# Kernel tuning notes

Hardware: AMD Instinct MI355X
Metric: run time of the kernel (lower is better)

## Reference

```python
import jax, jax.numpy as jnp
import numpy as np

H = 128      # hidden_dim
D = 256      # 2*hidden_dim (transformer d_model)
NH = 4       # attention heads
EPS = 1e-5

def _bn(x, g, b):
    # BatchNorm1d, training mode: batch statistics over node axis (biased var)
    mu = x.mean(0)
    var = x.var(0)
    return (x - mu) / jnp.sqrt(var + EPS) * g + b

def _ln(x, g, b):
    mu = x.mean(-1, keepdims=True)
    var = x.var(-1, keepdims=True)
    return (x - mu) / jnp.sqrt(var + EPS) * g + b

def _sage(x_src, x_dst, src, dst, Wl, bl, Wr):
    # PyG SAGEConv(aggr='mean'): lin_l(mean_j x_src[src_j]) + lin_r(x_dst); lin_r has no bias
    n_dst = x_dst.shape[0]
    msg = x_src[src]  # [E, H] gather
    agg = jnp.zeros((n_dst, msg.shape[-1]), msg.dtype).at[dst].add(msg)
    cnt = jnp.zeros((n_dst,), msg.dtype).at[dst].add(1.0)
    agg = agg / jnp.maximum(cnt, 1.0)[:, None]
    return agg @ Wl + bl + x_dst @ Wr


def setup_inputs() -> dict:
    key = jax.random.key(0)
    T, NU, NT, FU, FT = 12, 10000, 2500, 64, 32
    E_tt, E_ut, E_tu = 50000, 100000, 100000
    L, TL, FFN = 3, 3, 256
    ks = iter(jax.random.split(key, 64))
    def nrm(shape, s=0.05):
        return jax.random.normal(next(ks), shape, jnp.float32) * s
    inp = {
        'x_user': nrm((T, NU, FU), 1.0),
        'x_tag': nrm((T, NT, FT), 1.0),
        'edge_tt': jax.random.randint(next(ks), (T, 2, E_tt), 0, NT),
        'edge_ut_src': jax.random.randint(next(ks), (T, E_ut), 0, NU),
        'edge_ut_dst': jax.random.randint(next(ks), (T, E_ut), 0, NT),
        'edge_tu_src': jax.random.randint(next(ks), (T, E_tu), 0, NT),
        'edge_tu_dst': jax.random.randint(next(ks), (T, E_tu), 0, NU),
        'bn_user_g': jnp.ones((FU,)), 'bn_user_b': jnp.zeros((FU,)),
        'bn_tag_g': jnp.ones((FT,)), 'bn_tag_b': jnp.zeros((FT,)),
        'proj_user_W': nrm((FU, H)), 'proj_user_b': jnp.zeros((H,)),
        'proj_tag_W': nrm((FT, H)), 'proj_tag_b': jnp.zeros((H,)),
        # conv params: axis0 = conv layer (3), axis1 = edge type (0:tt, 1:ut, 2:tu)
        'conv_Wl': nrm((L, 3, H, H)), 'conv_bl': jnp.zeros((L, 3, H)),
        'conv_Wr': nrm((L, 3, H, H)),
        'attn_Wq': nrm((TL, D, D)), 'attn_bq': jnp.zeros((TL, D)),
        'attn_Wk': nrm((TL, D, D)), 'attn_bk': jnp.zeros((TL, D)),
        'attn_Wv': nrm((TL, D, D)), 'attn_bv': jnp.zeros((TL, D)),
        'attn_Wo': nrm((TL, D, D)), 'attn_bo': jnp.zeros((TL, D)),
        'ln1_g': jnp.ones((TL, D)), 'ln1_b': jnp.zeros((TL, D)),
        'ffn_W1': nrm((TL, D, FFN)), 'ffn_b1': jnp.zeros((TL, FFN)),
        'ffn_W2': nrm((TL, FFN, D)), 'ffn_b2': jnp.zeros((TL, D)),
        'ln2_g': jnp.ones((TL, D)), 'ln2_b': jnp.zeros((TL, D)),
        'head_W': nrm((D, 4)), 'head_b': jnp.zeros((4,)),
    }
    return inp


def reference(x_user, x_tag, edge_tt, edge_ut_src, edge_ut_dst, edge_tu_src, edge_tu_dst,
              bn_user_g, bn_user_b, bn_tag_g, bn_tag_b,
              proj_user_W, proj_user_b, proj_tag_W, proj_tag_b,
              conv_Wl, conv_bl, conv_Wr,
              attn_Wq, attn_bq, attn_Wk, attn_bk, attn_Wv, attn_bv, attn_Wo, attn_bo,
              ln1_g, ln1_b, ffn_W1, ffn_b1, ffn_W2, ffn_b2, ln2_g, ln2_b,
              head_W, head_b):
    def month(xu, xt, e_tt, eus, eud, ets, etd):
        xu = _bn(xu, bn_user_g, bn_user_b) @ proj_user_W + proj_user_b
        xt = _bn(xt, bn_tag_g, bn_tag_b) @ proj_tag_W + proj_tag_b
        for l in range(conv_Wl.shape[0]):
            o_tt = _sage(xt, xt, e_tt[0], e_tt[1], conv_Wl[l, 0], conv_bl[l, 0], conv_Wr[l, 0])
            o_ut = _sage(xu, xt, eus, eud, conv_Wl[l, 1], conv_bl[l, 1], conv_Wr[l, 1])
            o_tu = _sage(xt, xu, ets, etd, conv_Wl[l, 2], conv_bl[l, 2], conv_Wr[l, 2])
            # HeteroConv aggr='mean': tag receives 2 relations, user receives 1
            xt = jax.nn.relu((o_tt + o_ut) * 0.5)
            xu = jax.nn.relu(o_tu)
        return jnp.concatenate([xu.mean(0), xt.mean(0)])  # [2H]

    emb = jax.vmap(month)(x_user, x_tag, edge_tt, edge_ut_src, edge_ut_dst,
                          edge_tu_src, edge_tu_dst)  # [12, 2H]
    x = emb[None]  # [1, 12, D]
    B, S, Dm = x.shape
    dh = Dm // NH
    scale = 1.0 / jnp.sqrt(jnp.float32(dh))
    for l in range(attn_Wq.shape[0]):
        q = (x @ attn_Wq[l] + attn_bq[l]).reshape(B, S, NH, dh)
        k = (x @ attn_Wk[l] + attn_bk[l]).reshape(B, S, NH, dh)
        v = (x @ attn_Wv[l] + attn_bv[l]).reshape(B, S, NH, dh)
        a = jax.nn.softmax(jnp.einsum('bqhd,bkhd->bhqk', q, k) * scale, axis=-1)
        o = jnp.einsum('bhqk,bkhd->bqhd', a, v).reshape(B, S, Dm) @ attn_Wo[l] + attn_bo[l]
        x = _ln(x + o, ln1_g[l], ln1_b[l])          # post-norm (norm_first=False)
        f = jax.nn.relu(x @ ffn_W1[l] + ffn_b1[l]) @ ffn_W2[l] + ffn_b2[l]
        x = _ln(x + f, ln2_g[l], ln2_b[l])
    # predictions: columns = [qpd, answer_rate, retention, growth]
    return x[:, -1, :] @ head_W + head_b  # [1, 4]
```

## Files before the change

### kernel.cpp

```cpp
#include <hip/hip_runtime.h>

constexpr int T = 12;
constexpr int NU = 10000;
constexpr int NT = 2500;
constexpr int FU = 64;
constexpr int FT = 32;
constexpr int H = 128;
constexpr int D = 256;
constexpr int E_TT = 50000;
constexpr int E_UT = 100000;
constexpr int E_TU = 100000;
constexpr float EPS = 1e-5f;

__global__ __launch_bounds__(256) void bnsum_kernel(
    const float* __restrict__ x, int N, int F, float* __restrict__ sum,
    float* __restrict__ sq, int bpm) {
  int m = blockIdx.x / bpm, bc = blockIdx.x % bpm;
  int g = 256 / F;
  int c = threadIdx.x % F, rg = threadIdx.x / F;
  int rows = (N + bpm - 1) / bpm;
  int lo = bc * rows, hi = min(N, lo + rows);
  float s = 0.f, q = 0.f;
  for (int r = lo + rg; r < hi; r += g) {
    float v = x[((long)m * N + r) * F + c];
    s += v; q += v * v;
  }
  __shared__ float ssm[256], qsm[256];
  ssm[threadIdx.x] = s; qsm[threadIdx.x] = q;
  __syncthreads();
  if (rg == 0) {
    for (int i = 1; i < g; ++i) { s += ssm[i * F + c]; q += qsm[i * F + c]; }
    atomicAdd(&sum[m * F + c], s);
    atomicAdd(&sq[m * F + c], q);
  }
}

template <int F>
__global__ __launch_bounds__(128) void proj_kernel(
    const float* __restrict__ x, const float* __restrict__ sum, const float* __restrict__ sq,
    const float* __restrict__ g, const float* __restrict__ b,
    const float* __restrict__ W, const float* __restrict__ pb,
    float* __restrict__ out, int N, int chunks) {
  constexpr int RPB = 8;
  int m = blockIdx.x / chunks, chunk = blockIdx.x % chunks;
  int row0 = chunk * RPB;
  int nr = min(RPB, N - row0);
  int c = threadIdx.x;
  __shared__ __align__(16) float Ws[F][H];
  __shared__ __align__(16) float A[RPB][F];
  __shared__ float scv[F], shv[F];
  for (int k = 0; k < F; ++k) Ws[k][c] = W[k * H + c];
  if (c < F) {
    float mu = sum[m * F + c] * (1.f / N);
    float var = sq[m * F + c] * (1.f / N) - mu * mu;
    float inv = rsqrtf(var + EPS);
    float s = g[c] * inv;
    scv[c] = s; shv[c] = b[c] - mu * s;
  }
  __syncthreads();
  const float* xb = x + ((long)m * N + row0) * F;
  for (int i = c; i < nr * F; i += 128) {
    int kk = i % F;
    A[i / F][kk] = xb[i] * scv[kk] + shv[kk];
  }
  __syncthreads();
  float acc[RPB];
#pragma unroll
  for (int r = 0; r < RPB; ++r) acc[r] = 0.f;
  for (int k = 0; k < F; k += 4) {
    float w0 = Ws[k][c], w1 = Ws[k + 1][c], w2 = Ws[k + 2][c], w3 = Ws[k + 3][c];
#pragma unroll
    for (int r = 0; r < RPB; ++r) {
      float4 a = *(const float4*)&A[r][k];
      acc[r] += a.x * w0 + a.y * w1 + a.z * w2 + a.w * w3;
    }
  }
  float bias = pb[c];
  float* ob = out + ((long)m * N + row0) * H;
  for (int r = 0; r < nr; ++r) ob[r * H + c] = acc[r] + bias;
}

__global__ __launch_bounds__(256) void count_kernel(
    const int* __restrict__ dst, long mstride, int E, int* __restrict__ cnt, int N) {
  long idx = (long)blockIdx.x * 256 + threadIdx.x;
  if (idx >= (long)T * E) return;
  int m = (int)(idx / E), e = (int)(idx % E);
  int d = dst[m * mstride + e];
  atomicAdd(&cnt[m * N + d], 1);
}

__global__ __launch_bounds__(1024) void scan_kernel(
    int* __restrict__ iw, long cnt_tt, long off_tt, long cur_tt,
    long cnt_ut, long off_ut, long cur_ut,
    long cnt_tu, long off_tu, long cur_tu) {
  int b = blockIdx.x;
  int type = b / 12, m = b % 12;
  const int* cnt; int* off; int* cur; int N;
  if (type == 0) {
    cnt = iw + cnt_tt + (long)m * NT; off = iw + off_tt + (long)m * (NT + 1);
    cur = iw + cur_tt + (long)m * NT; N = NT;
  } else if (type == 1) {
    cnt = iw + cnt_ut + (long)m * NT; off = iw + off_ut + (long)m * (NT + 1);
    cur = iw + cur_ut + (long)m * NT; N = NT;
  } else {
    cnt = iw + cnt_tu + (long)m * NU; off = iw + off_tu + (long)m * (NU + 1);
    cur = iw + cur_tu + (long)m * NU; N = NU;
  }
  __shared__ int s[1024];
  int tid = threadIdx.x;
  int running = 0;
  for (int base = 0; base < N; base += 1024) {
    int i = base + tid;
    int v = (i < N) ? cnt[i] : 0;
    s[tid] = v;
    __syncthreads();
    for (int o = 1; o < 1024; o <<= 1) {
      int t = (tid >= o) ? s[tid - o] : 0;
      __syncthreads();
      s[tid] += t;
      __syncthreads();
    }
    if (i < N) { int e = running + s[tid] - v; off[i] = e; cur[i] = e; }
    int tot = s[1023];
    __syncthreads();
    running += tot;
  }
  if (tid == 0) off[N] = running;
}

__global__ __launch_bounds__(256) void fill_kernel(
    const int* __restrict__ src, long sstride, const int* __restrict__ dst, long dstride,
    int E, int* __restrict__ cur, int N, int* __restrict__ srcs) {
  long idx = (long)blockIdx.x * 256 + threadIdx.x;
  if (idx >= (long)T * E) return;
  int m = (int)(idx / E), e = (int)(idx % E);
  int d = dst[m * dstride + e];
  int sv = src[m * sstride + e];
  int pos = atomicAdd(&cur[m * N + d], 1);
  srcs[(long)m * E + pos] = sv;
}

__global__ __launch_bounds__(256) void agg_kernel(
    const int* __restrict__ off, const int* __restrict__ srcs,
    const float* __restrict__ xsrc, float* __restrict__ agg,
    int Ndst, int Nsrc, int E, int chunks) {
  int m = blockIdx.x / chunks, chunk = blockIdx.x % chunks;
  int slot = threadIdx.x >> 5;
  int c4 = (threadIdx.x & 31) * 4;
  int row = chunk * 8 + slot;
  if (row >= Ndst) return;
  const int* o = off + (long)m * (Ndst + 1);
  int o0 = o[row], o1 = o[row + 1];
  const int* sp = srcs + (long)m * E;
  const float* xb = xsrc + (long)m * Nsrc * H;
  float4 acc = {0.f, 0.f, 0.f, 0.f};
  for (int j = o0; j < o1; ++j) {
    float4 v = *(const float4*)&xb[(long)sp[j] * H + c4];
    acc.x += v.x; acc.y += v.y; acc.z += v.z; acc.w += v.w;
  }
  float inv = 1.f / (float)max(o1 - o0, 1);
  acc.x *= inv; acc.y *= inv; acc.z *= inv; acc.w *= inv;
  *(float4*)&agg[((long)m * Ndst + row) * H + c4] = acc;
}

__global__ __launch_bounds__(128) void update_tag_kernel(
    float* __restrict__ xt, const float* __restrict__ aggtt, const float* __restrict__ aggut,
    const float* __restrict__ Wl, const float* __restrict__ bl, const float* __restrict__ Wr,
    int layer, int chunks) {
  constexpr int RPB = 16;
  int m = blockIdx.x / chunks, chunk = blockIdx.x % chunks;
  int row0 = chunk * RPB;
  int nr = min(RPB, NT - row0);
  int c = threadIdx.x;
  __shared__ __align__(16) float sm0[RPB][H], sm1[RPB][H], sm2[RPB][H];
  const float* p0 = aggtt + ((long)m * NT + row0) * H;
  const float* p1 = xt + ((long)m * NT + row0) * H;
  const float* p2 = aggut + ((long)m * NT + row0) * H;
  for (int r = 0; r < nr; ++r) {
    sm0[r][c] = p0[r * H + c];
    sm1[r][c] = p1[r * H + c];
    sm2[r][c] = p2[r * H + c];
  }
  __syncthreads();
  const float* wl0 = Wl + (long)(layer * 3 + 0) * H * H;
  const float* wr0 = Wr + (long)(layer * 3 + 0) * H * H;
  const float* wl1 = Wl + (long)(layer * 3 + 1) * H * H;
  const float* wr1 = Wr + (long)(layer * 3 + 1) * H * H;
  float acc[RPB];
#pragma unroll
  for (int r = 0; r < RPB; ++r) acc[r] = 0.f;
  for (int k = 0; k < H; k += 4) {
    float a0[4], a1[4], a2[4];
#pragma unroll
    for (int u = 0; u < 4; ++u) {
      a0[u] = wl0[(k + u) * H + c];
      a1[u] = wr0[(k + u) * H + c] + wr1[(k + u) * H + c];
      a2[u] = wl1[(k + u) * H + c];
    }
#pragma unroll
    for (int r = 0; r < RPB; ++r) {
      float4 v0 = *(const float4*)&sm0[r][k];
      float4 v1 = *(const float4*)&sm1[r][k];
      float4 v2 = *(const float4*)&sm2[r][k];
      acc[r] += v0.x * a0[0] + v0.y * a0[1] + v0.z * a0[2] + v0.w * a0[3]
              + v1.x * a1[0] + v1.y * a1[1] + v1.z * a1[2] + v1.w * a1[3]
              + v2.x * a2[0] + v2.y * a2[1] + v2.z * a2[2] + v2.w * a2[3];
    }
  }
  float bias = bl[(layer * 3 + 0) * H + c] + bl[(layer * 3 + 1) * H + c];
  float* ob = xt + ((long)m * NT + row0) * H;
  for (int r = 0; r < nr; ++r) ob[r * H + c] = fmaxf(0.f, 0.5f * (acc[r] + bias));
}

__global__ __launch_bounds__(128) void update_user_kernel(
    float* __restrict__ xu, const float* __restrict__ aggtu,
    const float* __restrict__ Wl, const float* __restrict__ bl, const float* __restrict__ Wr,
    int layer, int chunks) {
  constexpr int RPB = 16;
  int m = blockIdx.x / chunks, chunk = blockIdx.x % chunks;
  int row0 = chunk * RPB;
  int nr = min(RPB, NU - row0);
  int c = threadIdx.x;
  __shared__ __align__(16) float sm0[RPB][H], sm1[RPB][H];
  const float* p0 = aggtu + ((long)m * NU + row0) * H;
  const float* p1 = xu + ((long)m * NU + row0) * H;
  for (int r = 0; r < nr; ++r) {
    sm0[r][c] = p0[r * H + c];
    sm1[r][c] = p1[r * H + c];
  }
  __syncthreads();
  const float* wl = Wl + (long)(layer * 3 + 2) * H * H;
  const float* wr = Wr + (long)(layer * 3 + 2) * H * H;
  float acc[RPB];
#pragma unroll
  for (int r = 0; r < RPB; ++r) acc[r] = 0.f;
  for (int k = 0; k < H; k += 4) {
    float a0[4], a1[4];
#pragma unroll
    for (int u = 0; u < 4; ++u) {
      a0[u] = wl[(k + u) * H + c];
      a1[u] = wr[(k + u) * H + c];
    }
#pragma unroll
    for (int r = 0; r < RPB; ++r) {
      float4 v0 = *(const float4*)&sm0[r][k];
      float4 v1 = *(const float4*)&sm1[r][k];
      acc[r] += v0.x * a0[0] + v0.y * a0[1] + v0.z * a0[2] + v0.w * a0[3]
              + v1.x * a1[0] + v1.y * a1[1] + v1.z * a1[2] + v1.w * a1[3];
    }
  }
  float bias = bl[(layer * 3 + 2) * H + c];
  float* ob = xu + ((long)m * NU + row0) * H;
  for (int r = 0; r < nr; ++r) ob[r * H + c] = fmaxf(0.f, acc[r] + bias);
}

__global__ __launch_bounds__(256) void pool_kernel(
    const float* __restrict__ x, int N, float* __restrict__ emb, int base, int bpm) {
  int m = blockIdx.x / bpm, bc = blockIdx.x % bpm;
  int c = threadIdx.x & 127, rg = threadIdx.x >> 7;
  int rows = (N + bpm - 1) / bpm;
  int lo = bc * rows, hi = min(N, lo + rows);
  float acc = 0.f;
  for (int r = lo + rg; r < hi; r += 2) acc += x[((long)m * N + r) * H + c];
  __shared__ float smem[2][H];
  smem[rg][c] = acc;
  __syncthreads();
  if (threadIdx.x < H) {
    atomicAdd(&emb[m * D + base + c], (smem[0][c] + smem[1][c]) * (1.f / N));
  }
}

__device__ __forceinline__ void fma4(float4& a, const float4 x, const float4 w0,
                                     const float4 w1, const float4 w2, const float4 w3) {
  a.x += x.x * w0.x + x.y * w1.x + x.z * w2.x + x.w * w3.x;
  a.y += x.x * w0.y + x.y * w1.y + x.z * w2.y + x.w * w3.y;
  a.z += x.x * w0.z + x.y * w1.z + x.z * w2.z + x.w * w3.z;
  a.w += x.x * w0.w + x.y * w1.w + x.z * w2.w + x.w * w3.w;
}

__device__ __forceinline__ void mm_slice(const float (&Xs)[12][256], const float* __restrict__ W,
                                         int ks, int tid, float* __restrict__ pOut) {
  int cg = tid & 63, rg = tid >> 6;
  int c4 = cg * 4;
  int s0 = rg * 3;
  float4 a0 = {0, 0, 0, 0}, a1 = {0, 0, 0, 0}, a2 = {0, 0, 0, 0};
  for (int k = ks * 64; k < ks * 64 + 64; k += 4) {
    float4 w0 = *(const float4*)&W[(k + 0) * 256 + c4];
    float4 w1 = *(const float4*)&W[(k + 1) * 256 + c4];
    float4 w2 = *(const float4*)&W[(k + 2) * 256 + c4];
    float4 w3 = *(const float4*)&W[(k + 3) * 256 + c4];
    fma4(a0, *(const float4*)&Xs[s0 + 0][k], w0, w1, w2, w3);
    fma4(a1, *(const float4*)&Xs[s0 + 1][k], w0, w1, w2, w3);
    fma4(a2, *(const float4*)&Xs[s0 + 2][k], w0, w1, w2, w3);
  }
  *(float4*)&pOut[(s0 + 0) * 256 + c4] = a0;
  *(float4*)&pOut[(s0 + 1) * 256 + c4] = a1;
  *(float4*)&pOut[(s0 + 2) * 256 + c4] = a2;
}

__device__ __forceinline__ void ln_rows(float (&Xs)[12][256], const float* __restrict__ g,
                                        const float* __restrict__ b, float (&rs)[4],
                                        float (&rq)[4], int tid) {
  for (int s = 0; s < 12; ++s) {
    float v = Xs[s][tid];
    float sm_ = v, sq_ = v * v;
    for (int o = 32; o > 0; o >>= 1) {
      sm_ += __shfl_down(sm_, o);
      sq_ += __shfl_down(sq_, o);
    }
    if ((tid & 63) == 0) { rs[tid >> 6] = sm_; rq[tid >> 6] = sq_; }
    __syncthreads();
    float mu = (rs[0] + rs[1] + rs[2] + rs[3]) * (1.f / 256);
    float var = (rq[0] + rq[1] + rq[2] + rq[3]) * (1.f / 256) - mu * mu;
    Xs[s][tid] = (v - mu) * rsqrtf(var + EPS) * g[tid] + b[tid];
    __syncthreads();
  }
}

__global__ __launch_bounds__(256) void trans_qkv(
    const float* __restrict__ xb, const float* __restrict__ pF2, const float* __restrict__ x1v,
    const float* __restrict__ b2, const float* __restrict__ ln2g, const float* __restrict__ ln2b,
    float* __restrict__ xb_out,
    const float* __restrict__ Wq, const float* __restrict__ Wk, const float* __restrict__ Wv,
    float* __restrict__ pQKV, int fuse) {
  __shared__ float Xs[12][256];
  __shared__ float rs[4], rq[4];
  int tid = threadIdx.x;
  int mat = blockIdx.x >> 2, ks = blockIdx.x & 3;
  if (fuse) {
    for (int s = 0; s < 12; ++s) {
      int i = s * 256 + tid;
      Xs[s][tid] = pF2[i] + pF2[3072 + i] + pF2[6144 + i] + pF2[9216 + i] + b2[tid] + x1v[i];
    }
    __syncthreads();
    ln_rows(Xs, ln2g, ln2b, rs, rq, tid);
    if (blockIdx.x == 0)
      for (int s = 0; s < 12; ++s) xb_out[s * 256 + tid] = Xs[s][tid];
  } else {
    for (int s = 0; s < 12; ++s) Xs[s][tid] = xb[s * 256 + tid];
    __syncthreads();
  }
  const float* W = (mat == 0) ? Wq : (mat == 1) ? Wk : Wv;
  mm_slice(Xs, W, ks, tid, pQKV + (mat * 4 + ks) * 3072);
}

__global__ __launch_bounds__(256) void trans_attn(
    const float* __restrict__ pQKV, const float* __restrict__ bq,
    const float* __restrict__ bk, const float* __restrict__ bv, float* __restrict__ O) {
  __shared__ float Qs[12][256], Ksh[12][256], Vs[12][256];
  __shared__ float Sc[4][12][12];
  int tid = threadIdx.x;
  for (int s = 0; s < 12; ++s) {
    int i = s * 256 + tid;
    const float* p = pQKV;
    Qs[s][tid] = p[i] + p[3072 + i] + p[6144 + i] + p[9216 + i] + bq[tid];
    p = pQKV + 12288;
    Ksh[s][tid] = p[i] + p[3072 + i] + p[6144 + i] + p[9216 + i] + bk[tid];
    p = pQKV + 24576;
    Vs[s][tid] = p[i] + p[3072 + i] + p[6144 + i] + p[9216 + i] + bv[tid];
  }
  __syncthreads();
  for (int idx = tid; idx < 576; idx += 256) {
    int h = idx / 144, rem = idx % 144, qi = rem / 12, ti = rem % 12;
    float acc = 0.f;
    for (int d = 0; d < 64; d += 4) {
      float4 qv = *(const float4*)&Qs[qi][h * 64 + d];
      float4 kv = *(const float4*)&Ksh[ti][h * 64 + d];
      acc += qv.x * kv.x + qv.y * kv.y + qv.z * kv.z + qv.w * kv.w;
    }
    Sc[h][qi][ti] = acc * 0.125f;
  }
  __syncthreads();
  if (tid < 48) {
    int h = tid / 12, qi = tid % 12;
    float mx = -1e30f;
    for (int t2 = 0; t2 < 12; ++t2) mx = fmaxf(mx, Sc[h][qi][t2]);
    float e[12], sum = 0.f;
    for (int t2 = 0; t2 < 12; ++t2) { e[t2] = __expf(Sc[h][qi][t2] - mx); sum += e[t2]; }
    float inv = 1.f / sum;
    for (int t2 = 0; t2 < 12; ++t2) Sc[h][qi][t2] = e[t2] * inv;
  }
  __syncthreads();
  int h = tid >> 6;
#pragma unroll
  for (int s = 0; s < 12; ++s) {
    float acc = 0.f;
#pragma unroll
    for (int t2 = 0; t2 < 12; ++t2) acc += Sc[h][s][t2] * Vs[t2][tid];
    O[s * 256 + tid] = acc;
  }
}

__global__ __launch_bounds__(256) void trans_mm(
    const float* __restrict__ In, const float* __restrict__ W, float* __restrict__ pOut) {
  __shared__ float Xs[12][256];
  int tid = threadIdx.x, ks = blockIdx.x;
  for (int s = 0; s < 12; ++s) Xs[s][tid] = In[s * 256 + tid];
  __syncthreads();
  mm_slice(Xs, W, ks, tid, pOut + ks * 3072);
}

__global__ __launch_bounds__(256) void trans_ffn1(
    const float* __restrict__ pP, const float* __restrict__ bo, const float* __restrict__ xb,
    const float* __restrict__ ln1g, const float* __restrict__ ln1b, float* __restrict__ x1_out,
    const float* __restrict__ W1, float* __restrict__ pF1) {
  __shared__ float Xs[12][256];
  __shared__ float rs[4], rq[4];
  int tid = threadIdx.x, ks = blockIdx.x;
  for (int s = 0; s < 12; ++s) {
    int i = s * 256 + tid;
    Xs[s][tid] = pP[i] + pP[3072 + i] + pP[6144 + i] + pP[9216 + i] + bo[tid] + xb[i];
  }
  __syncthreads();
  ln_rows(Xs, ln1g, ln1b, rs, rq, tid);
  if (ks == 0)
    for (int s = 0; s < 12; ++s) x1_out[s * 256 + tid] = Xs[s][tid];
  mm_slice(Xs, W1, ks, tid, pF1 + ks * 3072);
}

__global__ __launch_bounds__(256) void trans_ffn2(
    const float* __restrict__ pF1, const float* __restrict__ b1,
    const float* __restrict__ W2, float* __restrict__ pF2) {
  __shared__ float Xs[12][256];
  int tid = threadIdx.x, ks = blockIdx.x;
  for (int s = 0; s < 12; ++s) {
    int i = s * 256 + tid;
    Xs[s][tid] = fmaxf(0.f, pF1[i] + pF1[3072 + i] + pF1[6144 + i] + pF1[9216 + i] + b1[tid]);
  }
  __syncthreads();
  mm_slice(Xs, W2, ks, tid, pF2 + ks * 3072);
}

__global__ __launch_bounds__(256) void trans_head(
    const float* __restrict__ pF2, const float* __restrict__ b2, const float* __restrict__ x1v,
    const float* __restrict__ ln2g, const float* __restrict__ ln2b,
    const float* __restrict__ hW, const float* __restrict__ hb, float* __restrict__ out) {
  __shared__ float h[256];
  __shared__ float rs[4], rq[4];
  int tid = threadIdx.x;
  int i = 11 * 256 + tid;
  float v = pF2[i] + pF2[3072 + i] + pF2[6144 + i] + pF2[9216 + i] + b2[tid] + x1v[i];
  float sm_ = v, sq_ = v * v;
  for (int o = 32; o > 0; o >>= 1) { sm_ += __shfl_down(sm_, o); sq_ += __shfl_down(sq_, o); }
  if ((tid & 63) == 0) { rs[tid >> 6] = sm_; rq[tid >> 6] = sq_; }
  __syncthreads();
  float mu = (rs[0] + rs[1] + rs[2] + rs[3]) * (1.f / 256);
  float var = (rq[0] + rq[1] + rq[2] + rq[3]) * (1.f / 256) - mu * mu;
  h[tid] = (v - mu) * rsqrtf(var + EPS) * ln2g[tid] + ln2b[tid];
  __syncthreads();
  if (tid < 4) {
    float acc = hb[tid];
    for (int k = 0; k < 256; ++k) acc += h[k] * hW[k * 4 + tid];
    out[tid] = acc;
  }
}

extern "C" void kernel_launch(void* const* d_in, const int* in_sizes, int n_in,
                              void* d_out, int out_size, void* d_ws, size_t ws_size,
                              hipStream_t stream) {
  (void)in_sizes; (void)n_in; (void)out_size; (void)ws_size;
  const float* x_user = (const float*)d_in[0];
  const float* x_tag  = (const float*)d_in[1];
  const int* edge_tt  = (const int*)d_in[2];
  const int* e_us     = (const int*)d_in[3];
  const int* e_ud     = (const int*)d_in[4];
  const int* e_ts     = (const int*)d_in[5];
  const int* e_td     = (const int*)d_in[6];
  const float* bn_ug  = (const float*)d_in[7];
  const float* bn_ub  = (const float*)d_in[8];
  const float* bn_tg  = (const float*)d_in[9];
  const float* bn_tb  = (const float*)d_in[10];
  const float* pu_W   = (const float*)d_in[11];
  const float* pu_b   = (const float*)d_in[12];
  const float* pt_W   = (const float*)d_in[13];
  const float* pt_b   = (const float*)d_in[14];
  const float* cWl    = (const float*)d_in[15];
  const float* cbl    = (const float*)d_in[16];
  const float* cWr    = (const float*)d_in[17];
  const float* aWq    = (const float*)d_in[18];
  const float* abq    = (const float*)d_in[19];
  const float* aWk    = (const float*)d_in[20];
  const float* abk    = (const float*)d_in[21];
  const float* aWv    = (const float*)d_in[22];
  const float* abv    = (const float*)d_in[23];
  const float* aWo    = (const float*)d_in[24];
  const float* abo    = (const float*)d_in[25];
  const float* l1g    = (const float*)d_in[26];
  const float* l1b    = (const float*)d_in[27];
  const float* fW1    = (const float*)d_in[28];
  const float* fb1    = (const float*)d_in[29];
  const float* fW2    = (const float*)d_in[30];
  const float* fb2    = (const float*)d_in[31];
  const float* l2g    = (const float*)d_in[32];
  const float* l2b    = (const float*)d_in[33];
  const float* hW     = (const float*)d_in[34];
  const float* hb     = (const float*)d_in[35];

  float* ws = (float*)d_ws;
  int* iw = (int*)d_ws;
  size_t o = 0;
  auto alloc = [&](size_t n) { size_t r = o; o += n; return r; };
  size_t sum_u = alloc(T * FU), sq_u = alloc(T * FU);
  size_t sum_t = alloc(T * FT), sq_t = alloc(T * FT);
  size_t cnt_tt = alloc((size_t)T * NT), cnt_ut = alloc((size_t)T * NT), cnt_tu = alloc((size_t)T * NU);
  size_t emb = alloc(T * D);
  size_t zeroElems = o;
  size_t off_tt = alloc((size_t)T * (NT + 1)), off_ut = alloc((size_t)T * (NT + 1)), off_tu = alloc((size_t)T * (NU + 1));
  size_t cur_tt = alloc((size_t)T * NT), cur_ut = alloc((size_t)T * NT), cur_tu = alloc((size_t)T * NU);
  size_t srcs_tt = alloc((size_t)T * E_TT), srcs_ut = alloc((size_t)T * E_UT), srcs_tu = alloc((size_t)T * E_TU);
  size_t xu = alloc((size_t)T * NU * H), xt = alloc((size_t)T * NT * H);
  size_t agg_tt = alloc((size_t)T * NT * H), agg_ut = alloc((size_t)T * NT * H), agg_tu = alloc((size_t)T * NU * H);

  size_t pQKV = cnt_tt;
  size_t pP   = cnt_tt + 36864;
  size_t pF1  = cnt_tt + 49152;
  size_t pF2  = cnt_tt + 61440;
  size_t Ob   = cnt_tt + 73728;
  size_t x1b  = cnt_tt + 76800;

  hipMemsetAsync(d_ws, 0, zeroElems * sizeof(float), stream);

  bnsum_kernel<<<dim3(T * 8), 256, 0, stream>>>(x_user, NU, FU, ws + sum_u, ws + sq_u, 8);
  bnsum_kernel<<<dim3(T * 4), 256, 0, stream>>>(x_tag, NT, FT, ws + sum_t, ws + sq_t, 4);
  proj_kernel<FU><<<dim3(T * ((NU + 7) / 8)), 128, 0, stream>>>(
      x_user, ws + sum_u, ws + sq_u, bn_ug, bn_ub, pu_W, pu_b, ws + xu, NU, (NU + 7) / 8);
  proj_kernel<FT><<<dim3(T * ((NT + 7) / 8)), 128, 0, stream>>>(
      x_tag, ws + sum_t, ws + sq_t, bn_tg, bn_tb, pt_W, pt_b, ws + xt, NT, (NT + 7) / 8);
  count_kernel<<<dim3((T * E_TT + 255) / 256), 256, 0, stream>>>(edge_tt + E_TT, 2L * E_TT, E_TT, iw + cnt_tt, NT);
  count_kernel<<<dim3((T * E_UT + 255) / 256), 256, 0, stream>>>(e_ud, E_UT, E_UT, iw + cnt_ut, NT);
  count_kernel<<<dim3((T * E_TU + 255) / 256), 256, 0, stream>>>(e_td, E_TU, E_TU, iw + cnt_tu, NU);
  scan_kernel<<<dim3(36), 1024, 0, stream>>>(iw, (long)cnt_tt, (long)off_tt, (long)cur_tt,
                                             (long)cnt_ut, (long)off_ut, (long)cur_ut,
                                             (long)cnt_tu, (long)off_tu, (long)cur_tu);
  fill_kernel<<<dim3((T * E_TT + 255) / 256), 256, 0, stream>>>(edge_tt, 2L * E_TT, edge_tt + E_TT, 2L * E_TT, E_TT, iw + cur_tt, NT, iw + srcs_tt);
  fill_kernel<<<dim3((T * E_UT + 255) / 256), 256, 0, stream>>>(e_us, E_UT, e_ud, E_UT, E_UT, iw + cur_ut, NT, iw + srcs_ut);
  fill_kernel<<<dim3((T * E_TU + 255) / 256), 256, 0, stream>>>(e_ts, E_TU, e_td, E_TU, E_TU, iw + cur_tu, NU, iw + srcs_tu);
  int ch_t = (NT + 7) / 8, ch_u = (NU + 7) / 8;
  for (int l = 0; l < 3; ++l) {
    agg_kernel<<<dim3(T * ch_t), 256, 0, stream>>>(iw + off_tt, iw + srcs_tt, ws + xt, ws + agg_tt, NT, NT, E_TT, ch_t);
    agg_kernel<<<dim3(T * ch_t), 256, 0, stream>>>(iw + off_ut, iw + srcs_ut, ws + xu, ws + agg_ut, NT, NU, E_UT, ch_t);
    agg_kernel<<<dim3(T * ch_u), 256, 0, stream>>>(iw + off_tu, iw + srcs_tu, ws + xt, ws + agg_tu, NU, NT, E_TU, ch_u);
    update_tag_kernel<<<dim3(T * ((NT + 15) / 16)), 128, 0, stream>>>(ws + xt, ws + agg_tt, ws + agg_ut, cWl, cbl, cWr, l, (NT + 15) / 16);
    update_user_kernel<<<dim3(T * ((NU + 15) / 16)), 128, 0, stream>>>(ws + xu, ws + agg_tu, cWl, cbl, cWr, l, (NU + 15) / 16);
  }
  pool_kernel<<<dim3(T * 8), 256, 0, stream>>>(ws + xu, NU, ws + emb, 0, 8);
  pool_kernel<<<dim3(T * 2), 256, 0, stream>>>(ws + xt, NT, ws + emb, H, 2);
  long DD = (long)D * D;
  for (int l = 0; l < 3; ++l) {
    int fuse = (l > 0);
    int lp = fuse ? (l - 1) : 0;
    trans_qkv<<<dim3(12), 256, 0, stream>>>(
        ws + emb, ws + pF2, ws + x1b, fb2 + lp * D, l2g + lp * D, l2b + lp * D, ws + emb,
        aWq + l * DD, aWk + l * DD, aWv + l * DD, ws + pQKV, fuse);
    trans_attn<<<dim3(1), 256, 0, stream>>>(ws + pQKV, abq + l * D, abk + l * D, abv + l * D, ws + Ob);
    trans_mm<<<dim3(4), 256, 0, stream>>>(ws + Ob, aWo + l * DD, ws + pP);
    trans_ffn1<<<dim3(4), 256, 0, stream>>>(ws + pP, abo + l * D, ws + emb, l1g + l * D, l1b + l * D,
                                            ws + x1b, fW1 + l * DD, ws + pF1);
    trans_ffn2<<<dim3(4), 256, 0, stream>>>(ws + pF1, fb1 + l * D, fW2 + l * DD, ws + pF2);
  }
  trans_head<<<dim3(1), 256, 0, stream>>>(ws + pF2, fb2 + 2 * D, ws + x1b, l2g + 2 * D, l2b + 2 * D,
                                          hW, hb, (float*)d_out);
}
```

Before: 2.683 ms.

## Use 4x4 register tiles in projection and SAGE update GEMMs, unroll gathers

The per-node projection and SAGE update kernels move from one output column per thread over many rows to 4x4 register tiles with float4 weight loads read straight from global memory, and blocks grow to 256 threads covering 32 rows. The tt and ut root weights are pre-summed once by a new combine kernel. The neighbour gather loop is unrolled by four with independent accumulators, and pooling uses float4 loads with more blocks. The aim is more arithmetic per load and fewer shared-memory reads per FMA. In exchange, weight reads now depend on L1/L2 caching and the workspace layout shifts to hold the combined weights.

```diff
diff --git a/kernel.cpp b/kernel.cpp
--- a/kernel.cpp
+++ b/kernel.cpp
@@ -11,6 +11,17 @@
 constexpr int E_UT = 100000;
 constexpr int E_TU = 100000;
 constexpr float EPS = 1e-5f;
+
+__device__ __forceinline__ void fma4(float4& a, const float4 x, const float4 w0,
+                                     const float4 w1, const float4 w2, const float4 w3) {
+  a.x += x.x * w0.x + x.y * w1.x + x.z * w2.x + x.w * w3.x;
+  a.y += x.x * w0.y + x.y * w1.y + x.z * w2.y + x.w * w3.y;
+  a.z += x.x * w0.z + x.y * w1.z + x.z * w2.z + x.w * w3.z;
+  a.w += x.x * w0.w + x.y * w1.w + x.z * w2.w + x.w * w3.w;
+}
+__device__ __forceinline__ void add4(float4& a, const float4 v) {
+  a.x += v.x; a.y += v.y; a.z += v.z; a.w += v.w;
+}
 
 __global__ __launch_bounds__(256) void bnsum_kernel(
     const float* __restrict__ x, int N, int F, float* __restrict__ sum,
@@ -36,48 +47,61 @@
 }
 
 template <int F>
-__global__ __launch_bounds__(128) void proj_kernel(
+__global__ __launch_bounds__(256) void proj_kernel(
     const float* __restrict__ x, const float* __restrict__ sum, const float* __restrict__ sq,
     const float* __restrict__ g, const float* __restrict__ b,
     const float* __restrict__ W, const float* __restrict__ pb,
     float* __restrict__ out, int N, int chunks) {
-  constexpr int RPB = 8;
+  constexpr int RPB = 32;
+  constexpr int KG = F / 4;
   int m = blockIdx.x / chunks, chunk = blockIdx.x % chunks;
   int row0 = chunk * RPB;
   int nr = min(RPB, N - row0);
-  int c = threadIdx.x;
-  __shared__ __align__(16) float Ws[F][H];
+  int tid = threadIdx.x;
+  int cg = tid & 31, rg = tid >> 5;
+  int c4 = cg * 4, r0 = rg * 4;
   __shared__ __align__(16) float A[RPB][F];
-  __shared__ float scv[F], shv[F];
-  for (int k = 0; k < F; ++k) Ws[k][c] = W[k * H + c];
-  if (c < F) {
-    float mu = sum[m * F + c] * (1.f / N);
-    float var = sq[m * F + c] * (1.f / N) - mu * mu;
+  __shared__ __align__(16) float scv[F], shv[F];
+  if (tid < F) {
+    float mu = sum[m * F + tid] * (1.f / N);
+    float var = sq[m * F + tid] * (1.f / N) - mu * mu;
     float inv = rsqrtf(var + EPS);
-    float s = g[c] * inv;
-    scv[c] = s; shv[c] = b[c] - mu * s;
+    float s = g[tid] * inv;
+    scv[tid] = s; shv[tid] = b[tid] - mu * s;
   }
   __syncthreads();
   const float* xb = x + ((long)m * N + row0) * F;
-  for (int i = c; i < nr * F; i += 128) {
-    int kk = i % F;
-    A[i / F][kk] = xb[i] * scv[kk] + shv[kk];
-  }
-  __syncthreads();
-  float acc[RPB];
-#pragma unroll
-  for (int r = 0; r < RPB; ++r) acc[r] = 0.f;
+  for (int i = tid; i < nr * KG; i += 256) {
+    int r = i / KG, k4 = (i % KG) * 4;
+    float4 xv = *(const float4*)&xb[r * F + k4];
+    float4 s4 = *(const float4*)&scv[k4];
+    float4 h4 = *(const float4*)&shv[k4];
+    float4 a;
+    a.x = xv.x * s4.x + h4.x; a.y = xv.y * s4.y + h4.y;
+    a.z = xv.z * s4.z + h4.z; a.w = xv.w * s4.w + h4.w;
+    *(float4*)&A[r][k4] = a;
+  }
+  __syncthreads();
+  float4 acc[4] = {{0,0,0,0},{0,0,0,0},{0,0,0,0},{0,0,0,0}};
   for (int k = 0; k < F; k += 4) {
-    float w0 = Ws[k][c], w1 = Ws[k + 1][c], w2 = Ws[k + 2][c], w3 = Ws[k + 3][c];
-#pragma unroll
-    for (int r = 0; r < RPB; ++r) {
-      float4 a = *(const float4*)&A[r][k];
-      acc[r] += a.x * w0 + a.y * w1 + a.z * w2 + a.w * w3;
-    }
-  }
-  float bias = pb[c];
+    float4 w0 = *(const float4*)&W[(k + 0) * H + c4];
+    float4 w1 = *(const float4*)&W[(k + 1) * H + c4];
+    float4 w2 = *(const float4*)&W[(k + 2) * H + c4];
+    float4 w3 = *(const float4*)&W[(k + 3) * H + c4];
+#pragma unroll
+    for (int r = 0; r < 4; ++r)
+      fma4(acc[r], *(const float4*)&A[r0 + r][k], w0, w1, w2, w3);
+  }
+  float4 bias = *(const float4*)&pb[c4];
   float* ob = out + ((long)m * N + row0) * H;
-  for (int r = 0; r < nr; ++r) ob[r * H + c] = acc[r] + bias;
+#pragma unroll
+  for (int r = 0; r < 4; ++r)
+    if (r0 + r < nr) {
+      float4 o4;
+      o4.x = acc[r].x + bias.x; o4.y = acc[r].y + bias.y;
+      o4.z = acc[r].z + bias.z; o4.w = acc[r].w + bias.w;
+      *(float4*)&ob[(r0 + r) * H + c4] = o4;
+    }
 }
 
 __global__ __launch_bounds__(256) void count_kernel(
@@ -140,6 +164,13 @@
   srcs[(long)m * E + pos] = sv;
 }
 
+__global__ __launch_bounds__(256) void combine_wr_kernel(
+    const float* __restrict__ Wr, float* __restrict__ wrc) {
+  int i = blockIdx.x * 256 + threadIdx.x;
+  int l = i / (H * H), j = i % (H * H);
+  wrc[i] = Wr[(long)(l * 3 + 0) * H * H + j] + Wr[(long)(l * 3 + 1) * H * H + j];
+}
+
 __global__ __launch_bounds__(256) void agg_kernel(
     const int* __restrict__ off, const int* __restrict__ srcs,
     const float* __restrict__ xsrc, float* __restrict__ agg,
@@ -153,129 +184,156 @@
   int o0 = o[row], o1 = o[row + 1];
   const int* sp = srcs + (long)m * E;
   const float* xb = xsrc + (long)m * Nsrc * H;
-  float4 acc = {0.f, 0.f, 0.f, 0.f};
-  for (int j = o0; j < o1; ++j) {
-    float4 v = *(const float4*)&xb[(long)sp[j] * H + c4];
-    acc.x += v.x; acc.y += v.y; acc.z += v.z; acc.w += v.w;
-  }
+  float4 a0 = {0,0,0,0}, a1 = {0,0,0,0}, a2 = {0,0,0,0}, a3 = {0,0,0,0};
+  int j = o0;
+  for (; j + 3 < o1; j += 4) {
+    int s0 = sp[j], s1 = sp[j + 1], s2 = sp[j + 2], s3 = sp[j + 3];
+    add4(a0, *(const float4*)&xb[(long)s0 * H + c4]);
+    add4(a1, *(const float4*)&xb[(long)s1 * H + c4]);
+    add4(a2, *(const float4*)&xb[(long)s2 * H + c4]);
+    add4(a3, *(const float4*)&xb[(long)s3 * H + c4]);
+  }
+  for (; j < o1; ++j) add4(a0, *(const float4*)&xb[(long)sp[j] * H + c4]);
+  add4(a0, a1); add4(a2, a3); add4(a0, a2);
   float inv = 1.f / (float)max(o1 - o0, 1);
-  acc.x *= inv; acc.y *= inv; acc.z *= inv; acc.w *= inv;
-  *(float4*)&agg[((long)m * Ndst + row) * H + c4] = acc;
-}
-
-__global__ __launch_bounds__(128) void update_tag_kernel(
+  a0.x *= inv; a0.y *= inv; a0.z *= inv; a0.w *= inv;
+  *(float4*)&agg[((long)m * Ndst + row) * H + c4] = a0;
+}
+
+__global__ __launch_bounds__(256) void update_tag_kernel(
     float* __restrict__ xt, const float* __restrict__ aggtt, const float* __restrict__ aggut,
-    const float* __restrict__ Wl, const float* __restrict__ bl, const float* __restrict__ Wr,
+    const float* __restrict__ Wl, const float* __restrict__ bl, const float* __restrict__ wrc,
     int layer, int chunks) {
-  constexpr int RPB = 16;
   int m = blockIdx.x / chunks, chunk = blockIdx.x % chunks;
-  int row0 = chunk * RPB;
-  int nr = min(RPB, NT - row0);
-  int c = threadIdx.x;
-  __shared__ __align__(16) float sm0[RPB][H], sm1[RPB][H], sm2[RPB][H];
+  int row0 = chunk * 32;
+  int nr = min(32, NT - row0);
+  int tid = threadIdx.x;
+  int cg = tid & 31, rg = tid >> 5;
+  int c4 = cg * 4, r0 = rg * 4;
+  __shared__ __align__(16) float sm0[32][H], sm1[32][H], sm2[32][H];
   const float* p0 = aggtt + ((long)m * NT + row0) * H;
   const float* p1 = xt + ((long)m * NT + row0) * H;
   const float* p2 = aggut + ((long)m * NT + row0) * H;
-  for (int r = 0; r < nr; ++r) {
-    sm0[r][c] = p0[r * H + c];
-    sm1[r][c] = p1[r * H + c];
-    sm2[r][c] = p2[r * H + c];
+  for (int i = tid; i < nr * 32; i += 256) {
+    int r = i >> 5, k4 = (i & 31) * 4;
+    *(float4*)&sm0[r][k4] = *(const float4*)&p0[r * H + k4];
+    *(float4*)&sm1[r][k4] = *(const float4*)&p1[r * H + k4];
+    *(float4*)&sm2[r][k4] = *(const float4*)&p2[r * H + k4];
   }
   __syncthreads();
   const float* wl0 = Wl + (long)(layer * 3 + 0) * H * H;
-  const float* wr0 = Wr + (long)(layer * 3 + 0) * H * H;
   const float* wl1 = Wl + (long)(layer * 3 + 1) * H * H;
-  const float* wr1 = Wr + (long)(layer * 3 + 1) * H * H;
-  float acc[RPB];
-#pragma unroll
-  for (int r = 0; r < RPB; ++r) acc[r] = 0.f;
+  const float* wc = wrc + (long)layer * H * H;
+  float4 acc[4] = {{0,0,0,0},{0,0,0,0},{0,0,0,0},{0,0,0,0}};
   for (int k = 0; k < H; k += 4) {
-    float a0[4], a1[4], a2[4];
-#pragma unroll
-    for (int u = 0; u < 4; ++u) {
-      a0[u] = wl0[(k + u) * H + c];
-      a1[u] = wr0[(k + u) * H + c] + wr1[(k + u) * H + c];
-      a2[u] = wl1[(k + u) * H + c];
-    }
-#pragma unroll
-    for (int r = 0; r < RPB; ++r) {
-      float4 v0 = *(const float4*)&sm0[r][k];
-      float4 v1 = *(const float4*)&sm1[r][k];
-      float4 v2 = *(const float4*)&sm2[r][k];
-      acc[r] += v0.x * a0[0] + v0.y * a0[1] + v0.z * a0[2] + v0.w * a0[3]
-              + v1.x * a1[0] + v1.y * a1[1] + v1.z * a1[2] + v1.w * a1[3]
-              + v2.x * a2[0] + v2.y * a2[1] + v2.z * a2[2] + v2.w * a2[3];
-    }
-  }
-  float bias = bl[(layer * 3 + 0) * H + c] + bl[(layer * 3 + 1) * H + c];
+    float4 u0 = *(const float4*)&wl0[(k + 0) * H + c4];
+    float4 u1 = *(const float4*)&wl0[(k + 1) * H + c4];
+    float4 u2 = *(const float4*)&wl0[(k + 2) * H + c4];
+    float4 u3 = *(const float4*)&wl0[(k + 3) * H + c4];
+    float4 v0 = *(const float4*)&wc[(k + 0) * H + c4];
+    float4 v1 = *(const float4*)&wc[(k + 1) * H + c4];
+    float4 v2 = *(const float4*)&wc[(k + 2) * H + c4];
+    float4 v3 = *(const float4*)&wc[(k + 3) * H + c4];
+    float4 t0 = *(const float4*)&wl1[(k + 0) * H + c4];
+    float4 t1 = *(const float4*)&wl1[(k + 1) * H + c4];
+    float4 t2 = *(const float4*)&wl1[(k + 2) * H + c4];
+    float4 t3 = *(const float4*)&wl1[(k + 3) * H + c4];
+#pragma unroll
+    for (int r = 0; r < 4; ++r) {
+      fma4(acc[r], *(const float4*)&sm0[r0 + r][k], u0, u1, u2, u3);
+      fma4(acc[r], *(const float4*)&sm1[r0 + r][k], v0, v1, v2, v3);
+      fma4(acc[r], *(const float4*)&sm2[r0 + r][k], t0, t1, t2, t3);
+    }
+  }
+  float4 b0 = *(const float4*)&bl[(long)(layer * 3 + 0) * H + c4];
+  float4 b1 = *(const float4*)&bl[(long)(layer * 3 + 1) * H + c4];
   float* ob = xt + ((long)m * NT + row0) * H;
-  for (int r = 0; r < nr; ++r) ob[r * H + c] = fmaxf(0.f, 0.5f * (acc[r] + bias));
-}
-
-__global__ __launch_bounds__(128) void update_user_kernel(
+#pragma unroll
+  for (int r = 0; r < 4; ++r)
+    if (r0 + r < nr) {
+      float4 o4;
+      o4.x = fmaxf(0.f, 0.5f * (acc[r].x + b0.x + b1.x));
+      o4.y = fmaxf(0.f, 0.5f * (acc[r].y + b0.y + b1.y));
+      o4.z = fmaxf(0.f, 0.5f * (acc[r].z + b0.z + b1.z));
+      o4.w = fmaxf(0.f, 0.5f * (acc[r].w + b0.w + b1.w));
+      *(float4*)&ob[(r0 + r) * H + c4] = o4;
+    }
+}
+
+__global__ __launch_bounds__(256) void update_user_kernel(
     float* __restrict__ xu, const float* __restrict__ aggtu,
     const float* __restrict__ Wl, const float* __restrict__ bl, const float* __restrict__ Wr,
     int layer, int chunks) {
-  constexpr int RPB = 16;
   int m = blockIdx.x / chunks, chunk = blockIdx.x % chunks;
-  int row0 = chunk * RPB;
-  int nr = min(RPB, NU - row0);
-  int c = threadIdx.x;
-  __shared__ __align__(16) float sm0[RPB][H], sm1[RPB][H];
+  int row0 = chunk * 32;
+  int nr = min(32, NU - row0);
+  int tid = threadIdx.x;
+  int cg = tid & 31, rg = tid >> 5;
+  int c4 = cg * 4, r0 = rg * 4;
+  __shared__ __align__(16) float sm0[32][H], sm1[32][H];
   const float* p0 = aggtu + ((long)m * NU + row0) * H;
   const float* p1 = xu + ((long)m * NU + row0) * H;
-  for (int r = 0; r < nr; ++r) {
-    sm0[r][c] = p0[r * H + c];
-    sm1[r][c] = p1[r * H + c];
+  for (int i = tid; i < nr * 32; i += 256) {
+    int r = i >> 5, k4 = (i & 31) * 4;
+    *(float4*)&sm0[r][k4] = *(const float4*)&p0[r * H + k4];
+    *(float4*)&sm1[r][k4] = *(const float4*)&p1[r * H + k4];
   }
   __syncthreads();
   const float* wl = Wl + (long)(layer * 3 + 2) * H * H;
   const float* wr = Wr + (long)(layer * 3 + 2) * H * H;
-  float acc[RPB];
-#pragma unroll
-  for (int r = 0; r < RPB; ++r) acc[r] = 0.f;
+  float4 acc[4] = {{0,0,0,0},{0,0,0,0},{0,0,0,0},{0,0,0,0}};
   for (int k = 0; k < H; k += 4) {
-    float a0[4], a1[4];
-#pragma unroll
-    for (int u = 0; u < 4; ++u) {
-      a0[u] = wl[(k + u) * H + c];
-      a1[u] = wr[(k + u) * H + c];
-    }
-#pragma unroll
-    for (int r = 0; r < RPB; ++r) {
-      float4 v0 = *(const float4*)&sm0[r][k];
-      float4 v1 = *(const float4*)&sm1[r][k];
-      acc[r] += v0.x * a0[0] + v0.y * a0[1] + v0.z * a0[2] + v0.w * a0[3]
-              + v1.x * a1[0] + v1.y * a1[1] + v1.z * a1[2] + v1.w * a1[3];
-    }
-  }
-  float bias = bl[(layer * 3 + 2) * H + c];
+    float4 u0 = *(const float4*)&wl[(k + 0) * H + c4];
+    float4 u1 = *(const float4*)&wl[(k + 1) * H + c4];
+    float4 u2 = *(const float4*)&wl[(k + 2) * H + c4];
+    float4 u3 = *(const float4*)&wl[(k + 3) * H + c4];
+    float4 v0 = *(const float4*)&wr[(k + 0) * H + c4];
+    float4 v1 = *(const float4*)&wr[(k + 1) * H + c4];
+    float4 v2 = *(const float4*)&wr[(k + 2) * H + c4];
+    float4 v3 = *(const float4*)&wr[(k + 3) * H + c4];
+#pragma unroll
+    for (int r = 0; r < 4; ++r) {
+      fma4(acc[r], *(const float4*)&sm0[r0 + r][k], u0, u1, u2, u3);
+      fma4(acc[r], *(const float4*)&sm1[r0 + r][k], v0, v1, v2, v3);
+    }
+  }
+  float4 bias = *(const float4*)&bl[(long)(layer * 3 + 2) * H + c4];
   float* ob = xu + ((long)m * NU + row0) * H;
-  for (int r = 0; r < nr; ++r) ob[r * H + c] = fmaxf(0.f, acc[r] + bias);
+#pragma unroll
+  for (int r = 0; r < 4; ++r)
+    if (r0 + r < nr) {
+      float4 o4;
+      o4.x = fmaxf(0.f, acc[r].x + bias.x);
+      o4.y = fmaxf(0.f, acc[r].y + bias.y);
+      o4.z = fmaxf(0.f, acc[r].z + bias.z);
+      o4.w = fmaxf(0.f, acc[r].w + bias.w);
+      *(float4*)&ob[(r0 + r) * H + c4] = o4;
+    }
 }
 
 __global__ __launch_bounds__(256) void pool_kernel(
     const float* __restrict__ x, int N, float* __restrict__ emb, int base, int bpm) {
   int m = blockIdx.x / bpm, bc = blockIdx.x % bpm;
-  int c = threadIdx.x & 127, rg = threadIdx.x >> 7;
+  int cg = threadIdx.x & 31, rg = threadIdx.x >> 5;
+  int c4 = cg * 4;
   int rows = (N + bpm - 1) / bpm;
   int lo = bc * rows, hi = min(N, lo + rows);
-  float acc = 0.f;
-  for (int r = lo + rg; r < hi; r += 2) acc += x[((long)m * N + r) * H + c];
-  __shared__ float smem[2][H];
-  smem[rg][c] = acc;
-  __syncthreads();
-  if (threadIdx.x < H) {
-    atomicAdd(&emb[m * D + base + c], (smem[0][c] + smem[1][c]) * (1.f / N));
-  }
-}
-
-__device__ __forceinline__ void fma4(float4& a, const float4 x, const float4 w0,
-                                     const float4 w1, const float4 w2, const float4 w3) {
-  a.x += x.x * w0.x + x.y * w1.x + x.z * w2.x + x.w * w3.x;
-  a.y += x.x * w0.y + x.y * w1.y + x.z * w2.y + x.w * w3.y;
-  a.z += x.x * w0.z + x.y * w1.z + x.z * w2.z + x.w * w3.z;
-  a.w += x.x * w0.w + x.y * w1.w + x.z * w2.w + x.w * w3.w;
+  float4 acc = {0,0,0,0};
+  for (int r = lo + rg; r < hi; r += 8)
+    add4(acc, *(const float4*)&x[((long)m * N + r) * H + c4]);
+  __shared__ __align__(16) float4 sm[8][32];
+  sm[rg][cg] = acc;
+  __syncthreads();
+  if (rg == 0) {
+    float4 s = sm[0][cg];
+#pragma unroll
+    for (int i = 1; i < 8; ++i) add4(s, sm[i][cg]);
+    float inv = 1.f / (float)N;
+    atomicAdd(&emb[m * D + base + c4 + 0], s.x * inv);
+    atomicAdd(&emb[m * D + base + c4 + 1], s.y * inv);
+    atomicAdd(&emb[m * D + base + c4 + 2], s.z * inv);
+    atomicAdd(&emb[m * D + base + c4 + 3], s.w * inv);
+  }
 }
 
 __device__ __forceinline__ void mm_slice(const float (&Xs)[12][256], const float* __restrict__ W,
@@ -511,40 +569,44 @@
   size_t xu = alloc((size_t)T * NU * H), xt = alloc((size_t)T * NT * H);
   size_t agg_tt = alloc((size_t)T * NT * H), agg_ut = alloc((size_t)T * NT * H), agg_tu = alloc((size_t)T * NU * H);
 
-  size_t pQKV = cnt_tt;
-  size_t pP   = cnt_tt + 36864;
-  size_t pF1  = cnt_tt + 49152;
-  size_t pF2  = cnt_tt + 61440;
-  size_t Ob   = cnt_tt + 73728;
-  size_t x1b  = cnt_tt + 76800;
-
-  hipMemsetAsync(d_ws, 0, zeroElems * sizeof(float), stream);
+  size_t wrc  = cnt_tt;
+  size_t pQKV = cnt_tt + 49152;
+  size_t pP   = cnt_tt + 86016;
+  size_t pF1  = cnt_tt + 98304;
+  size_t pF2  = cnt_tt + 110592;
+  size_t Ob   = cnt_tt + 122880;
+  size_t x1b  = cnt_tt + 125952;
+
+  (void)hipMemsetAsync(d_ws, 0, zeroElems * sizeof(float), stream);
 
   bnsum_kernel<<<dim3(T * 8), 256, 0, stream>>>(x_user, NU, FU, ws + sum_u, ws + sq_u, 8);
   bnsum_kernel<<<dim3(T * 4), 256, 0, stream>>>(x_tag, NT, FT, ws + sum_t, ws + sq_t, 4);
-  proj_kernel<FU><<<dim3(T * ((NU + 7) / 8)), 128, 0, stream>>>(
-      x_user, ws + sum_u, ws + sq_u, bn_ug, bn_ub, pu_W, pu_b, ws + xu, NU, (NU + 7) / 8);
-  proj_kernel<FT><<<dim3(T * ((NT + 7) / 8)), 128, 0, stream>>>(
-      x_tag, ws + sum_t, ws + sq_t, bn_tg, bn_tb, pt_W, pt_b, ws + xt, NT, (NT + 7) / 8);
+  int pch_u = (NU + 31) / 32, pch_t = (NT + 31) / 32;
+  proj_kernel<FU><<<dim3(T * pch_u), 256, 0, stream>>>(
+      x_user, ws + sum_u, ws + sq_u, bn_ug, bn_ub, pu_W, pu_b, ws + xu, NU, pch_u);
+  proj_kernel<FT><<<dim3(T * pch_t), 256, 0, stream>>>(
+      x_tag, ws + sum_t, ws + sq_t, bn_tg, bn_tb, pt_W, pt_b, ws + xt, NT, pch_t);
   count_kernel<<<dim3((T * E_TT + 255) / 256), 256, 0, stream>>>(edge_tt + E_TT, 2L * E_TT, E_TT, iw + cnt_tt, NT);
   count_kernel<<<dim3((T * E_UT + 255) / 256), 256, 0, stream>>>(e_ud, E_UT, E_UT, iw + cnt_ut, NT);
   count_kernel<<<dim3((T * E_TU + 255) / 256), 256, 0, stream>>>(e_td, E_TU, E_TU, iw + cnt_tu, NU);
   scan_kernel<<<dim3(36), 1024, 0, stream>>>(iw, (long)cnt_tt, (long)off_tt, (long)cur_tt,
                                              (long)cnt_ut, (long)off_ut, (long)cur_ut,
                                              (long)cnt_tu, (long)off_tu, (long)cur_tu);
+  combine_wr_kernel<<<dim3(192), 256, 0, stream>>>(cWr, ws + wrc);
   fill_kernel<<<dim3((T * E_TT + 255) / 256), 256, 0, stream>>>(edge_tt, 2L * E_TT, edge_tt + E_TT, 2L * E_TT, E_TT, iw + cur_tt, NT, iw + srcs_tt);
   fill_kernel<<<dim3((T * E_UT + 255) / 256), 256, 0, stream>>>(e_us, E_UT, e_ud, E_UT, E_UT, iw + cur_ut, NT, iw + srcs_ut);
   fill_kernel<<<dim3((T * E_TU + 255) / 256), 256, 0, stream>>>(e_ts, E_TU, e_td, E_TU, E_TU, iw + cur_tu, NU, iw + srcs_tu);
-  int ch_t = (NT + 7) / 8, ch_u = (NU + 7) / 8;
+  int ach_t = (NT + 7) / 8, ach_u = (NU + 7) / 8;
+  int uch_t = (NT + 31) / 32, uch_u = (NU + 31) / 32;
   for (int l = 0; l < 3; ++l) {
-    agg_kernel<<<dim3(T * ch_t), 256, 0, stream>>>(iw + off_tt, iw + srcs_tt, ws + xt, ws + agg_tt, NT, NT, E_TT, ch_t);
-    agg_kernel<<<dim3(T * ch_t), 256, 0, stream>>>(iw + off_ut, iw + srcs_ut, ws + xu, ws + agg_ut, NT, NU, E_UT, ch_t);
-    agg_kernel<<<dim3(T * ch_u), 256, 0, stream>>>(iw + off_tu, iw + srcs_tu, ws + xt, ws + agg_tu, NU, NT, E_TU, ch_u);
-    update_tag_kernel<<<dim3(T * ((NT + 15) / 16)), 128, 0, stream>>>(ws + xt, ws + agg_tt, ws + agg_ut, cWl, cbl, cWr, l, (NT + 15) / 16);
-    update_user_kernel<<<dim3(T * ((NU + 15) / 16)), 128, 0, stream>>>(ws + xu, ws + agg_tu, cWl, cbl, cWr, l, (NU + 15) / 16);
-  }
-  pool_kernel<<<dim3(T * 8), 256, 0, stream>>>(ws + xu, NU, ws + emb, 0, 8);
-  pool_kernel<<<dim3(T * 2), 256, 0, stream>>>(ws + xt, NT, ws + emb, H, 2);
+    agg_kernel<<<dim3(T * ach_t), 256, 0, stream>>>(iw + off_tt, iw + srcs_tt, ws + xt, ws + agg_tt, NT, NT, E_TT, ach_t);
+    agg_kernel<<<dim3(T * ach_t), 256, 0, stream>>>(iw + off_ut, iw + srcs_ut, ws + xu, ws + agg_ut, NT, NU, E_UT, ach_t);
+    agg_kernel<<<dim3(T * ach_u), 256, 0, stream>>>(iw + off_tu, iw + srcs_tu, ws + xt, ws + agg_tu, NU, NT, E_TU, ach_u);
+    update_tag_kernel<<<dim3(T * uch_t), 256, 0, stream>>>(ws + xt, ws + agg_tt, ws + agg_ut, cWl, cbl, ws + wrc, l, uch_t);
+    update_user_kernel<<<dim3(T * uch_u), 256, 0, stream>>>(ws + xu, ws + agg_tu, cWl, cbl, cWr, l, uch_u);
+  }
+  pool_kernel<<<dim3(T * 16), 256, 0, stream>>>(ws + xu, NU, ws + emb, 0, 16);
+  pool_kernel<<<dim3(T * 8), 256, 0, stream>>>(ws + xt, NT, ws + emb, H, 8);
   long DD = (long)D * D;
   for (int l = 0; l < 3; ++l) {
     int fuse = (l > 0);
```

New measurement: 2.453 ms. -8.6%, faster.
